# Performance work log

Measured on AMD Instinct MI355X. Metric: run time of the kernel, lower is better.

## Reference

```python
import jax, jax.numpy as jnp
import numpy as np

B, T, D, NH = 2, 2048, 2048, 16
HID = D  # hidden_dim must equal emb_dim for the source's fc2(x1) to type-check
HD = D // NH
EPS = 1e-5


def setup_inputs() -> dict:
    key = jax.random.key(0)
    ks = jax.random.split(key, 16)
    s = 0.02
    inp = {
        "x": jax.random.normal(ks[0], (B, T, D), jnp.float32),
        "Wq": jax.random.normal(ks[1], (D, D), jnp.float32) * s,
        "bq": jnp.zeros((D,), jnp.float32),
        "Wk": jax.random.normal(ks[2], (D, D), jnp.float32) * s,
        "bk": jnp.zeros((D,), jnp.float32),
        "Wv": jax.random.normal(ks[3], (D, D), jnp.float32) * s,
        "bv": jnp.zeros((D,), jnp.float32),
        "Wo": jax.random.normal(ks[4], (D, D), jnp.float32) * s,
        "bo": jnp.zeros((D,), jnp.float32),
        "scale1": jnp.ones((D,), jnp.float32),
        "scale2": jnp.ones((D,), jnp.float32),
        "W1": jax.random.normal(ks[5], (D, HID), jnp.float32) * s,
        "W2": jax.random.normal(ks[6], (D, HID), jnp.float32) * s,  # fc2: Linear(emb_dim, hidden_dim)
        "W3": jax.random.normal(ks[7], (HID, D), jnp.float32) * s,
    }
    return inp


def _rmsnorm(x, scale):
    m = jnp.mean(x * x, axis=-1, keepdims=True)
    return scale * (x * jax.lax.rsqrt(m + EPS))


def _attention(x, Wq, bq, Wk, bk, Wv, bv, Wo, bo):
    b, t, _ = x.shape
    q = (x @ Wq + bq).reshape(b, t, NH, HD)
    k = (x @ Wk + bk).reshape(b, t, NH, HD)
    v = (x @ Wv + bv).reshape(b, t, NH, HD)
    # energy: [B, H, T, T]; softmax over keys, scaled by 1/sqrt(head_dim); NO causal mask in source
    energy = jnp.einsum("bqhd,bkhd->bhqk", q, k) / jnp.sqrt(jnp.float32(HD))
    attn = jax.nn.softmax(energy, axis=-1)
    out = jnp.einsum("bhqk,bkhd->bqhd", attn, v).reshape(b, t, D)
    return out @ Wo + bo


def _ffn(x, W1, W2, W3):
    x1 = x @ W1                       # [B,T,HID]
    x2 = x1 @ W2                      # source quirk: fc2 applied to x1 (hidden_dim == emb_dim)
    return (x1 * jax.nn.sigmoid(x1) * x2) @ W3


def reference(x, Wq, bq, Wk, bk, Wv, bv, Wo, bo, scale1, scale2, W1, W2, W3):
    shortcut = x
    h = _rmsnorm(x, scale1)
    h = _attention(h, Wq, bq, Wk, bk, Wv, bv, Wo, bo)
    h = shortcut + h
    h = _rmsnorm(h, scale2)
    h = _ffn(h, W1, W2, W3)
    # source adds the ORIGINAL input again (shortcut never reassigned)
    return h + shortcut
```

## Files before the change

### kernel.cpp

```cpp
#include <hip/hip_runtime.h>

typedef __bf16 bf16x8 __attribute__((ext_vector_type(8)));
typedef __bf16 bf16x4v __attribute__((ext_vector_type(4)));
typedef float  f32x4  __attribute__((ext_vector_type(4)));

#define LDS_AS(p) ((__attribute__((address_space(3))) void*)(p))
#define GLB_AS(p) ((const __attribute__((address_space(1))) void*)(p))

struct TP { const float* s[7]; __bf16* d[7]; };
__global__ __launch_bounds__(256) void transpose_convert_all(TP p) {
  const float* __restrict__ W = p.s[blockIdx.z];
  __bf16* __restrict__ Wt = p.d[blockIdx.z];
  __shared__ float tile[32][33];
  const int tx = threadIdx.x & 31, ty = threadIdx.x >> 5;
  const int n0 = blockIdx.x * 32, k0 = blockIdx.y * 32;
#pragma unroll
  for (int j = 0; j < 4; ++j)
    tile[ty + j * 8][tx] = W[(size_t)(k0 + ty + j * 8) * 2048 + n0 + tx];
  __syncthreads();
#pragma unroll
  for (int j = 0; j < 4; ++j)
    Wt[(size_t)(n0 + ty + j * 8) * 2048 + k0 + tx] = (__bf16)tile[tx][ty + j * 8];
}

__global__ __launch_bounds__(256) void rmsnorm_k(
    const float* __restrict__ x, const float* __restrict__ scale,
    __bf16* __restrict__ out) {
  const int row = blockIdx.x, t = threadIdx.x;
  const float4* xr = (const float4*)(x + (size_t)row * 2048);
  float4 a = xr[t], b2 = xr[t + 256];
  float ss = a.x * a.x + a.y * a.y + a.z * a.z + a.w * a.w +
             b2.x * b2.x + b2.y * b2.y + b2.z * b2.z + b2.w * b2.w;
#pragma unroll
  for (int ofs = 32; ofs; ofs >>= 1) ss += __shfl_xor(ss, ofs, 64);
  __shared__ float red[4];
  if ((t & 63) == 0) red[t >> 6] = ss;
  __syncthreads();
  ss = red[0] + red[1] + red[2] + red[3];
  const float rs = rsqrtf(ss * (1.f / 2048.f) + 1e-5f);
  const float4* sr = (const float4*)scale;
  float4 s1 = sr[t], s2 = sr[t + 256];
  __bf16* orow = out + (size_t)row * 2048;
  orow[t * 4 + 0] = (__bf16)(a.x * rs * s1.x);
  orow[t * 4 + 1] = (__bf16)(a.y * rs * s1.y);
  orow[t * 4 + 2] = (__bf16)(a.z * rs * s1.z);
  orow[t * 4 + 3] = (__bf16)(a.w * rs * s1.w);
  orow[(t + 256) * 4 + 0] = (__bf16)(b2.x * rs * s2.x);
  orow[(t + 256) * 4 + 1] = (__bf16)(b2.y * rs * s2.y);
  orow[(t + 256) * 4 + 2] = (__bf16)(b2.z * rs * s2.z);
  orow[(t + 256) * 4 + 3] = (__bf16)(b2.w * rs * s2.w);
}

template <bool OUTF32, bool HASBIAS, bool HASRES, bool SILU>
__global__ __launch_bounds__(256) void gemm_bt(
    const __bf16* __restrict__ A, const __bf16* __restrict__ Bt,
    const float* __restrict__ bias, const float* __restrict__ res,
    const __bf16* __restrict__ ew, void* __restrict__ Cout,
    int M, int N, int Kd) {
  __shared__ __attribute__((aligned(16))) __bf16 As[2][128 * 32];
  __shared__ __attribute__((aligned(16))) __bf16 Bs[2][128 * 32];
  const int tid = threadIdx.x;
  const int w = tid >> 6, l = tid & 63;
  const int M0 = blockIdx.y * 128, N0 = blockIdx.x * 128;
  const int wr = w >> 1, wc = w & 1;
  const int lm = l & 15, lq = l >> 4;

  f32x4 acc[4][4];
#pragma unroll
  for (int mt = 0; mt < 4; ++mt)
#pragma unroll
    for (int nt = 0; nt < 4; ++nt)
#pragma unroll
      for (int e = 0; e < 4; ++e) acc[mt][nt][e] = 0.f;

  const int offA0 = (w * 2 + 0) * 1024 + l * 16;
  const int offA1 = (w * 2 + 1) * 1024 + l * 16;
  const int row0 = offA0 >> 6, kb0 = offA0 & 63;
  const int row1 = offA1 >> 6, kb1 = offA1 & 63;
  const int nIt = Kd >> 5;

  auto stage = [&](int k0, int bsel) {
    const char* ga0 = (const char*)(A + (size_t)(M0 + row0) * Kd + k0) + kb0;
    const char* ga1 = (const char*)(A + (size_t)(M0 + row1) * Kd + k0) + kb1;
    const char* gb0 = (const char*)(Bt + (size_t)(N0 + row0) * Kd + k0) + kb0;
    const char* gb1 = (const char*)(Bt + (size_t)(N0 + row1) * Kd + k0) + kb1;
    __builtin_amdgcn_global_load_lds(GLB_AS(ga0), LDS_AS(((char*)As[bsel]) + (w * 2 + 0) * 1024), 16, 0, 0);
    __builtin_amdgcn_global_load_lds(GLB_AS(ga1), LDS_AS(((char*)As[bsel]) + (w * 2 + 1) * 1024), 16, 0, 0);
    __builtin_amdgcn_global_load_lds(GLB_AS(gb0), LDS_AS(((char*)Bs[bsel]) + (w * 2 + 0) * 1024), 16, 0, 0);
    __builtin_amdgcn_global_load_lds(GLB_AS(gb1), LDS_AS(((char*)Bs[bsel]) + (w * 2 + 1) * 1024), 16, 0, 0);
  };

  stage(0, 0);
  for (int it = 0; it < nIt; ++it) {
    __syncthreads();
    if (it + 1 < nIt) stage((it + 1) * 32, (it + 1) & 1);
    const __bf16* Ab = As[it & 1];
    const __bf16* Bb = Bs[it & 1];
    bf16x8 af[4], bfr[4];
#pragma unroll
    for (int mt = 0; mt < 4; ++mt)
      af[mt] = *(const bf16x8*)(Ab + (wr * 64 + mt * 16 + lm) * 32 + lq * 8);
#pragma unroll
    for (int nt = 0; nt < 4; ++nt)
      bfr[nt] = *(const bf16x8*)(Bb + (wc * 64 + nt * 16 + lm) * 32 + lq * 8);
#pragma unroll
    for (int mt = 0; mt < 4; ++mt)
#pragma unroll
      for (int nt = 0; nt < 4; ++nt)
        acc[mt][nt] = __builtin_amdgcn_mfma_f32_16x16x32_bf16(af[mt], bfr[nt], acc[mt][nt], 0, 0, 0);
  }

  const int lr = lq * 4;
#pragma unroll
  for (int mt = 0; mt < 4; ++mt) {
#pragma unroll
    for (int nt = 0; nt < 4; ++nt) {
      const int col = N0 + wc * 64 + nt * 16 + lm;
      float bv = 0.f;
      if (HASBIAS) bv = bias[col];
#pragma unroll
      for (int i = 0; i < 4; ++i) {
        const int row = M0 + wr * 64 + mt * 16 + lr + i;
        const size_t off = (size_t)row * N + col;
        float v = acc[mt][nt][i] + bv;
        if (HASRES) v += res[off];
        if (SILU) {
          const float x1v = (float)ew[off];
          v = x1v * (1.f / (1.f + __expf(-x1v))) * v;
        }
        if (OUTF32) ((float*)Cout)[off] = v;
        else ((__bf16*)Cout)[off] = (__bf16)v;
      }
    }
  }
}

__global__ __launch_bounds__(256) void gemm_qkv(
    const __bf16* __restrict__ A, const __bf16* __restrict__ Bt,
    const float* __restrict__ bq, const float* __restrict__ bk,
    const float* __restrict__ bv,
    __bf16* __restrict__ Qout, __bf16* __restrict__ Kout,
    __bf16* __restrict__ Vtout, int Kd) {
  __shared__ __attribute__((aligned(16))) __bf16 As[2][128 * 32];
  __shared__ __attribute__((aligned(16))) __bf16 Bs[2][128 * 32];
  const int tid = threadIdx.x;
  const int w = tid >> 6, l = tid & 63;
  const int M0 = blockIdx.y * 128, N0 = blockIdx.x * 128;
  const int wr = w >> 1, wc = w & 1;
  const int lm = l & 15, lq = l >> 4;

  f32x4 acc[4][4];
#pragma unroll
  for (int mt = 0; mt < 4; ++mt)
#pragma unroll
    for (int nt = 0; nt < 4; ++nt)
#pragma unroll
      for (int e = 0; e < 4; ++e) acc[mt][nt][e] = 0.f;

  const int offA0 = (w * 2 + 0) * 1024 + l * 16;
  const int offA1 = (w * 2 + 1) * 1024 + l * 16;
  const int row0 = offA0 >> 6, kb0 = offA0 & 63;
  const int row1 = offA1 >> 6, kb1 = offA1 & 63;
  const int nIt = Kd >> 5;

  auto stage = [&](int k0, int bsel) {
    const char* ga0 = (const char*)(A + (size_t)(M0 + row0) * Kd + k0) + kb0;
    const char* ga1 = (const char*)(A + (size_t)(M0 + row1) * Kd + k0) + kb1;
    const char* gb0 = (const char*)(Bt + (size_t)(N0 + row0) * Kd + k0) + kb0;
    const char* gb1 = (const char*)(Bt + (size_t)(N0 + row1) * Kd + k0) + kb1;
    __builtin_amdgcn_global_load_lds(GLB_AS(ga0), LDS_AS(((char*)As[bsel]) + (w * 2 + 0) * 1024), 16, 0, 0);
    __builtin_amdgcn_global_load_lds(GLB_AS(ga1), LDS_AS(((char*)As[bsel]) + (w * 2 + 1) * 1024), 16, 0, 0);
    __builtin_amdgcn_global_load_lds(GLB_AS(gb0), LDS_AS(((char*)Bs[bsel]) + (w * 2 + 0) * 1024), 16, 0, 0);
    __builtin_amdgcn_global_load_lds(GLB_AS(gb1), LDS_AS(((char*)Bs[bsel]) + (w * 2 + 1) * 1024), 16, 0, 0);
  };

  stage(0, 0);
  for (int it = 0; it < nIt; ++it) {
    __syncthreads();
    if (it + 1 < nIt) stage((it + 1) * 32, (it + 1) & 1);
    const __bf16* Ab = As[it & 1];
    const __bf16* Bb = Bs[it & 1];
    bf16x8 af[4], bfr[4];
#pragma unroll
    for (int mt = 0; mt < 4; ++mt)
      af[mt] = *(const bf16x8*)(Ab + (wr * 64 + mt * 16 + lm) * 32 + lq * 8);
#pragma unroll
    for (int nt = 0; nt < 4; ++nt)
      bfr[nt] = *(const bf16x8*)(Bb + (wc * 64 + nt * 16 + lm) * 32 + lq * 8);
#pragma unroll
    for (int mt = 0; mt < 4; ++mt)
#pragma unroll
      for (int nt = 0; nt < 4; ++nt)
        acc[mt][nt] = __builtin_amdgcn_mfma_f32_16x16x32_bf16(af[mt], bfr[nt], acc[mt][nt], 0, 0, 0);
  }

  const int lr = lq * 4;
  const int seg = N0 >> 11;
  const int nbase = N0 & 2047;
  const float* bb = (seg == 0) ? bq : ((seg == 1) ? bk : bv);
  if (seg < 2) {
    __bf16* dst = (seg == 0) ? Qout : Kout;
#pragma unroll
    for (int mt = 0; mt < 4; ++mt) {
#pragma unroll
      for (int nt = 0; nt < 4; ++nt) {
        const int col = nbase + wc * 64 + nt * 16 + lm;
        const float bvv = bb[col];
#pragma unroll
        for (int i = 0; i < 4; ++i) {
          const int row = M0 + wr * 64 + mt * 16 + lr + i;
          dst[(size_t)row * 2048 + col] = (__bf16)(acc[mt][nt][i] + bvv);
        }
      }
    }
  } else {
#pragma unroll
    for (int mt = 0; mt < 4; ++mt) {
#pragma unroll
      for (int nt = 0; nt < 4; ++nt) {
        const int col = nbase + wc * 64 + nt * 16 + lm;
        const float bvv = bb[col];
        const int rw0 = M0 + wr * 64 + mt * 16 + lr;
        const int bidx = rw0 >> 11, tok = rw0 & 2047;
        bf16x4v pk;
#pragma unroll
        for (int i = 0; i < 4; ++i) pk[i] = (__bf16)(acc[mt][nt][i] + bvv);
        *(bf16x4v*)(Vtout + ((size_t)(bidx * 2048 + col)) * 2048 + tok) = pk;
      }
    }
  }
}

__global__ __launch_bounds__(256, 2) void attn_mfma(
    const __bf16* __restrict__ Q, const __bf16* __restrict__ K,
    const __bf16* __restrict__ Vt, __bf16* __restrict__ O) {
  __shared__ __attribute__((aligned(16))) char KsL[2][16 * 1024];
  __shared__ __attribute__((aligned(16))) char VsL[2][16 * 1024];

  const int t = threadIdx.x;
  const int w = t >> 6, l = t & 63;
  const int lm = l & 15, quad = l >> 4;
  const int h = blockIdx.y, b = blockIdx.z;
  const int q0 = blockIdx.x * 128;
  const size_t Ds = 2048;
  const size_t hoff = (size_t)h * 128;
  const size_t bbase = (size_t)b * 2048;
  const int sl16 = ((lm << 2) | quad) * 16;
  const float SCL = 0.08838834764831845f * 1.4426950408889634f;

  const int krow = l >> 2, kcol = (l & 3) * 8;
  const int vth = l & 3, vd = l >> 2;

  bf16x8 qf[2][4];
#pragma unroll
  for (int ntq = 0; ntq < 2; ++ntq)
#pragma unroll
    for (int ks = 0; ks < 4; ++ks)
      qf[ntq][ks] = *(const bf16x8*)(Q + (bbase + q0 + w * 32 + ntq * 16 + lm) * Ds + hoff + ks * 32 + quad * 8);

  f32x4 oacc[2][8];
#pragma unroll
  for (int ntq = 0; ntq < 2; ++ntq)
#pragma unroll
    for (int nv = 0; nv < 8; ++nv)
#pragma unroll
      for (int e = 0; e < 4; ++e) oacc[ntq][nv][e] = 0.f;
  float lpart[2] = {0.f, 0.f};

  bf16x8 vreg[4];

  auto loadV = [&](int kt) {
#pragma unroll
    for (int i = 0; i < 4; ++i) {
      const int chunk = w * 4 + i;
      const int nv = chunk >> 1, c = chunk & 1;
      vreg[i] = *(const bf16x8*)(Vt + (bbase + hoff + nv * 16 + vd) * Ds + kt + c * 32 + vth * 8);
    }
  };
  auto stageK = [&](int kt, char* Kb) {
#pragma unroll
    for (int i = 0; i < 4; ++i) {
      const __bf16* src = K + (bbase + kt + i * 16 + krow) * Ds + hoff + w * 32 + kcol;
      __builtin_amdgcn_global_load_lds(GLB_AS(src), LDS_AS(Kb + (i * 4 + w) * 1024), 16, 0, 0);
    }
  };
  auto writeV = [&](char* Vb) {
    const int s0off = ((vd << 2) | ((vth & 1) * 2)) * 16 + (vth >> 1) * 8;
#pragma unroll
    for (int i = 0; i < 4; ++i) {
      char* base = Vb + (w * 4 + i) * 1024;
      uint4 u = *(const uint4*)&vreg[i];
      *(uint2*)(base + s0off) = make_uint2(u.x, u.y);
      *(uint2*)(base + s0off + 16) = make_uint2(u.z, u.w);
    }
  };

  loadV(0);
  stageK(0, KsL[0]);
  writeV(VsL[0]);

  for (int it = 0; it < 32; ++it) {
    __syncthreads();
    const int cur = it & 1;
    const bool more = (it + 1) < 32;
    if (more) { loadV((it + 1) * 64); stageK((it + 1) * 64, KsL[(it + 1) & 1]); }

    const char* Kb = KsL[cur];
    const char* Vb = VsL[cur];

    f32x4 st[4][2];
#pragma unroll
    for (int mtk = 0; mtk < 4; ++mtk)
#pragma unroll
      for (int ntq = 0; ntq < 2; ++ntq)
#pragma unroll
        for (int e = 0; e < 4; ++e) st[mtk][ntq][e] = 0.f;
#pragma unroll
    for (int ks = 0; ks < 4; ++ks) {
#pragma unroll
      for (int mtk = 0; mtk < 4; ++mtk) {
        bf16x8 kf = *(const bf16x8*)(Kb + (mtk * 4 + ks) * 1024 + sl16);
        st[mtk][0] = __builtin_amdgcn_mfma_f32_16x16x32_bf16(kf, qf[0][ks], st[mtk][0], 0, 0, 0);
        st[mtk][1] = __builtin_amdgcn_mfma_f32_16x16x32_bf16(kf, qf[1][ks], st[mtk][1], 0, 0, 0);
      }
    }

#pragma unroll
    for (int c = 0; c < 2; ++c) {
      bf16x8 pf[2];
#pragma unroll
      for (int ntq = 0; ntq < 2; ++ntq) {
#pragma unroll
        for (int half = 0; half < 2; ++half) {
          const f32x4 sv = st[c * 2 + half][ntq];
#pragma unroll
          for (int r = 0; r < 4; ++r) {
            const float p = exp2f(sv[r] * SCL);
            const __bf16 pb = (__bf16)p;
            pf[ntq][half * 4 + r] = pb;
            lpart[ntq] += (float)pb;
          }
        }
      }
#pragma unroll
      for (int nv = 0; nv < 8; ++nv) {
        bf16x8 vf = *(const bf16x8*)(Vb + (nv * 2 + c) * 1024 + sl16);
        oacc[0][nv] = __builtin_amdgcn_mfma_f32_16x16x32_bf16(pf[0], vf, oacc[0][nv], 0, 0, 0);
        oacc[1][nv] = __builtin_amdgcn_mfma_f32_16x16x32_bf16(pf[1], vf, oacc[1][nv], 0, 0, 0);
      }
    }

    if (more) writeV(VsL[(it + 1) & 1]);
  }

  float linv[2];
#pragma unroll
  for (int ntq = 0; ntq < 2; ++ntq) {
    float v = lpart[ntq];
    v += __shfl_xor(v, 16, 64);
    v += __shfl_xor(v, 32, 64);
    linv[ntq] = 1.f / v;
  }
  float oinv[2][4];
#pragma unroll
  for (int ntq = 0; ntq < 2; ++ntq)
#pragma unroll
    for (int r = 0; r < 4; ++r)
      oinv[ntq][r] = __shfl(linv[ntq], quad * 4 + r, 64);

#pragma unroll
  for (int ntq = 0; ntq < 2; ++ntq)
#pragma unroll
    for (int nv = 0; nv < 8; ++nv)
#pragma unroll
      for (int r = 0; r < 4; ++r) {
        const int qrow = q0 + w * 32 + ntq * 16 + quad * 4 + r;
        O[(bbase + qrow) * Ds + hoff + nv * 16 + lm] = (__bf16)(oacc[ntq][nv][r] * oinv[ntq][r]);
      }
}

extern "C" void kernel_launch(void* const* d_in, const int* in_sizes, int n_in,
                              void* d_out, int out_size, void* d_ws, size_t ws_size,
                              hipStream_t stream) {
  const float* x      = (const float*)d_in[0];
  const float* Wq     = (const float*)d_in[1];
  const float* bq     = (const float*)d_in[2];
  const float* Wk     = (const float*)d_in[3];
  const float* bk     = (const float*)d_in[4];
  const float* Wv     = (const float*)d_in[5];
  const float* bv     = (const float*)d_in[6];
  const float* Wo     = (const float*)d_in[7];
  const float* bo     = (const float*)d_in[8];
  const float* scale1 = (const float*)d_in[9];
  const float* scale2 = (const float*)d_in[10];
  const float* W1     = (const float*)d_in[11];
  const float* W2     = (const float*)d_in[12];
  const float* W3     = (const float*)d_in[13];

  const int M = 4096, N = 2048, Kd = 2048;
  char* ws = (char*)d_ws;
  const size_t WT_B = (size_t)2048 * 2048 * 2;
  const size_t ACT_B = (size_t)4096 * 2048 * 2;
  __bf16* wt[7];
  size_t off = 0;
  for (int i = 0; i < 7; ++i) { wt[i] = (__bf16*)(ws + off); off += WT_B; }
  __bf16* hn1  = (__bf16*)(ws + off); off += ACT_B;
  __bf16* Qb   = (__bf16*)(ws + off); off += ACT_B;
  __bf16* Kb   = (__bf16*)(ws + off); off += ACT_B;
  __bf16* VtG  = (__bf16*)(ws + off); off += ACT_B;
  __bf16* attn = (__bf16*)(ws + off); off += ACT_B;
  __bf16* hn2  = (__bf16*)(ws + off); off += ACT_B;
  __bf16* x1b  = (__bf16*)(ws + off); off += ACT_B;
  __bf16* fmb  = (__bf16*)(ws + off); off += ACT_B;

  dim3 tb(256);
  {
    TP p;
    p.s[0] = Wq; p.s[1] = Wk; p.s[2] = Wv; p.s[3] = Wo; p.s[4] = W1; p.s[5] = W2; p.s[6] = W3;
    for (int i = 0; i < 7; ++i) p.d[i] = wt[i];
    transpose_convert_all<<<dim3(64, 64, 7), tb, 0, stream>>>(p);
  }

  rmsnorm_k<<<4096, tb, 0, stream>>>(x, scale1, hn1);

  gemm_qkv<<<dim3(6144 / 128, M / 128), tb, 0, stream>>>(
      hn1, wt[0], bq, bk, bv, Qb, Kb, VtG, Kd);

  dim3 ag(2048 / 128, 16, 2);
  attn_mfma<<<ag, tb, 0, stream>>>(Qb, Kb, VtG, attn);

  dim3 gg(N / 128, M / 128);
  gemm_bt<true, true, true, false><<<gg, tb, 0, stream>>>(attn, wt[3], bo, x, nullptr, d_out, M, N, Kd);

  rmsnorm_k<<<4096, tb, 0, stream>>>((const float*)d_out, scale2, hn2);

  gemm_bt<false, false, false, false><<<gg, tb, 0, stream>>>(hn2, wt[4], nullptr, nullptr, nullptr, x1b, M, N, Kd);
  gemm_bt<false, false, false, true><<<gg, tb, 0, stream>>>(x1b, wt[5], nullptr, nullptr, x1b, fmb, M, N, Kd);
  gemm_bt<true, false, true, false><<<gg, tb, 0, stream>>>(fmb, wt[6], nullptr, x, nullptr, d_out, M, N, Kd);
}
```

Measured before the change: 649.2 us.

## Fold W1·W2 into one interleaved FFN GEMM with fused SiLU epilogue

Reassociates the FFN so that x2 = h·(W1·W2). A 2048³ weight GEMM computes W1·W2 on every call, and its columns are interleaved with W1 into a single 4096-wide B matrix. One GEMM then produces x1 and x2 tiles together and applies the SiLU gating in its epilogue through an LDS exchange, which removes the dependent second GEMM and the x1 round trip through global memory. The price is an extra weight GEMM plus an interleave copy, and x2 is now computed from a bf16-rounded W12, which slightly changes numerics. Separately, the QKV GEMM moves to 256x128 tiles with 4x8 MFMA accumulators per wave, to get more reuse of each B tile.

```diff
diff --git a/kernel.cpp b/kernel.cpp
--- a/kernel.cpp
+++ b/kernel.cpp
@@ -7,7 +7,7 @@
 #define LDS_AS(p) ((__attribute__((address_space(3))) void*)(p))
 #define GLB_AS(p) ((const __attribute__((address_space(1))) void*)(p))
 
-struct TP { const float* s[7]; __bf16* d[7]; };
+struct TP { const float* s[7]; __bf16* d[7]; __bf16* w1b; };
 __global__ __launch_bounds__(256) void transpose_convert_all(TP p) {
   const float* __restrict__ W = p.s[blockIdx.z];
   __bf16* __restrict__ Wt = p.d[blockIdx.z];
@@ -21,6 +21,21 @@
 #pragma unroll
   for (int j = 0; j < 4; ++j)
     Wt[(size_t)(n0 + ty + j * 8) * 2048 + k0 + tx] = (__bf16)tile[tx][ty + j * 8];
+  if (blockIdx.z == 4) {
+#pragma unroll
+    for (int j = 0; j < 4; ++j)
+      p.w1b[(size_t)(k0 + ty + j * 8) * 2048 + n0 + tx] = (__bf16)tile[ty + j * 8][tx];
+  }
+}
+
+__global__ __launch_bounds__(256) void ffn_interleave(
+    const __bf16* __restrict__ W1t, const __bf16* __restrict__ W12t,
+    __bf16* __restrict__ BtFFN) {
+  const int r = blockIdx.x;
+  const int t = r >> 7, c = r & 127;
+  const __bf16* src = (c < 64) ? (W1t + (size_t)(t * 64 + c) * 2048)
+                               : (W12t + (size_t)(t * 64 + (c - 64)) * 2048);
+  ((uint4*)(BtFFN + (size_t)r * 2048))[threadIdx.x] = ((const uint4*)src)[threadIdx.x];
 }
 
 __global__ __launch_bounds__(256) void rmsnorm_k(
@@ -51,12 +66,11 @@
   orow[(t + 256) * 4 + 3] = (__bf16)(b2.w * rs * s2.w);
 }
 
-template <bool OUTF32, bool HASBIAS, bool HASRES, bool SILU>
+template <bool OUTF32, bool HASBIAS, bool HASRES>
 __global__ __launch_bounds__(256) void gemm_bt(
     const __bf16* __restrict__ A, const __bf16* __restrict__ Bt,
     const float* __restrict__ bias, const float* __restrict__ res,
-    const __bf16* __restrict__ ew, void* __restrict__ Cout,
-    int M, int N, int Kd) {
+    void* __restrict__ Cout, int M, int N, int Kd) {
   __shared__ __attribute__((aligned(16))) __bf16 As[2][128 * 32];
   __shared__ __attribute__((aligned(16))) __bf16 Bs[2][128 * 32];
   const int tid = threadIdx.x;
@@ -73,21 +87,18 @@
 #pragma unroll
       for (int e = 0; e < 4; ++e) acc[mt][nt][e] = 0.f;
 
-  const int offA0 = (w * 2 + 0) * 1024 + l * 16;
-  const int offA1 = (w * 2 + 1) * 1024 + l * 16;
-  const int row0 = offA0 >> 6, kb0 = offA0 & 63;
-  const int row1 = offA1 >> 6, kb1 = offA1 & 63;
+  const int srow = l >> 2, sk = (l & 3) * 16;
   const int nIt = Kd >> 5;
 
   auto stage = [&](int k0, int bsel) {
-    const char* ga0 = (const char*)(A + (size_t)(M0 + row0) * Kd + k0) + kb0;
-    const char* ga1 = (const char*)(A + (size_t)(M0 + row1) * Kd + k0) + kb1;
-    const char* gb0 = (const char*)(Bt + (size_t)(N0 + row0) * Kd + k0) + kb0;
-    const char* gb1 = (const char*)(Bt + (size_t)(N0 + row1) * Kd + k0) + kb1;
-    __builtin_amdgcn_global_load_lds(GLB_AS(ga0), LDS_AS(((char*)As[bsel]) + (w * 2 + 0) * 1024), 16, 0, 0);
-    __builtin_amdgcn_global_load_lds(GLB_AS(ga1), LDS_AS(((char*)As[bsel]) + (w * 2 + 1) * 1024), 16, 0, 0);
-    __builtin_amdgcn_global_load_lds(GLB_AS(gb0), LDS_AS(((char*)Bs[bsel]) + (w * 2 + 0) * 1024), 16, 0, 0);
-    __builtin_amdgcn_global_load_lds(GLB_AS(gb1), LDS_AS(((char*)Bs[bsel]) + (w * 2 + 1) * 1024), 16, 0, 0);
+#pragma unroll
+    for (int i = 0; i < 2; ++i) {
+      const int c = w * 2 + i;
+      const char* ga = (const char*)(A + (size_t)(M0 + c * 16 + srow) * Kd + k0) + sk;
+      const char* gb = (const char*)(Bt + (size_t)(N0 + c * 16 + srow) * Kd + k0) + sk;
+      __builtin_amdgcn_global_load_lds(GLB_AS(ga), LDS_AS(((char*)As[bsel]) + c * 1024), 16, 0, 0);
+      __builtin_amdgcn_global_load_lds(GLB_AS(gb), LDS_AS(((char*)Bs[bsel]) + c * 1024), 16, 0, 0);
+    }
   };
 
   stage(0, 0);
@@ -124,10 +135,6 @@
         const size_t off = (size_t)row * N + col;
         float v = acc[mt][nt][i] + bv;
         if (HASRES) v += res[off];
-        if (SILU) {
-          const float x1v = (float)ew[off];
-          v = x1v * (1.f / (1.f + __expf(-x1v))) * v;
-        }
         if (OUTF32) ((float*)Cout)[off] = v;
         else ((__bf16*)Cout)[off] = (__bf16)v;
       }
@@ -141,37 +148,37 @@
     const float* __restrict__ bv,
     __bf16* __restrict__ Qout, __bf16* __restrict__ Kout,
     __bf16* __restrict__ Vtout, int Kd) {
-  __shared__ __attribute__((aligned(16))) __bf16 As[2][128 * 32];
+  __shared__ __attribute__((aligned(16))) __bf16 As[2][256 * 32];
   __shared__ __attribute__((aligned(16))) __bf16 Bs[2][128 * 32];
   const int tid = threadIdx.x;
   const int w = tid >> 6, l = tid & 63;
-  const int M0 = blockIdx.y * 128, N0 = blockIdx.x * 128;
-  const int wr = w >> 1, wc = w & 1;
+  const int M0 = blockIdx.y * 256, N0 = blockIdx.x * 128;
   const int lm = l & 15, lq = l >> 4;
 
-  f32x4 acc[4][4];
+  f32x4 acc[4][8];
 #pragma unroll
   for (int mt = 0; mt < 4; ++mt)
 #pragma unroll
-    for (int nt = 0; nt < 4; ++nt)
+    for (int nt = 0; nt < 8; ++nt)
 #pragma unroll
       for (int e = 0; e < 4; ++e) acc[mt][nt][e] = 0.f;
 
-  const int offA0 = (w * 2 + 0) * 1024 + l * 16;
-  const int offA1 = (w * 2 + 1) * 1024 + l * 16;
-  const int row0 = offA0 >> 6, kb0 = offA0 & 63;
-  const int row1 = offA1 >> 6, kb1 = offA1 & 63;
+  const int srow = l >> 2, sk = (l & 3) * 16;
   const int nIt = Kd >> 5;
 
   auto stage = [&](int k0, int bsel) {
-    const char* ga0 = (const char*)(A + (size_t)(M0 + row0) * Kd + k0) + kb0;
-    const char* ga1 = (const char*)(A + (size_t)(M0 + row1) * Kd + k0) + kb1;
-    const char* gb0 = (const char*)(Bt + (size_t)(N0 + row0) * Kd + k0) + kb0;
-    const char* gb1 = (const char*)(Bt + (size_t)(N0 + row1) * Kd + k0) + kb1;
-    __builtin_amdgcn_global_load_lds(GLB_AS(ga0), LDS_AS(((char*)As[bsel]) + (w * 2 + 0) * 1024), 16, 0, 0);
-    __builtin_amdgcn_global_load_lds(GLB_AS(ga1), LDS_AS(((char*)As[bsel]) + (w * 2 + 1) * 1024), 16, 0, 0);
-    __builtin_amdgcn_global_load_lds(GLB_AS(gb0), LDS_AS(((char*)Bs[bsel]) + (w * 2 + 0) * 1024), 16, 0, 0);
-    __builtin_amdgcn_global_load_lds(GLB_AS(gb1), LDS_AS(((char*)Bs[bsel]) + (w * 2 + 1) * 1024), 16, 0, 0);
+#pragma unroll
+    for (int i = 0; i < 4; ++i) {
+      const int c = w * 4 + i;
+      const char* ga = (const char*)(A + (size_t)(M0 + c * 16 + srow) * Kd + k0) + sk;
+      __builtin_amdgcn_global_load_lds(GLB_AS(ga), LDS_AS(((char*)As[bsel]) + c * 1024), 16, 0, 0);
+    }
+#pragma unroll
+    for (int i = 0; i < 2; ++i) {
+      const int c = w * 2 + i;
+      const char* gb = (const char*)(Bt + (size_t)(N0 + c * 16 + srow) * Kd + k0) + sk;
+      __builtin_amdgcn_global_load_lds(GLB_AS(gb), LDS_AS(((char*)Bs[bsel]) + c * 1024), 16, 0, 0);
+    }
   };
 
   stage(0, 0);
@@ -180,17 +187,17 @@
     if (it + 1 < nIt) stage((it + 1) * 32, (it + 1) & 1);
     const __bf16* Ab = As[it & 1];
     const __bf16* Bb = Bs[it & 1];
-    bf16x8 af[4], bfr[4];
-#pragma unroll
-    for (int mt = 0; mt < 4; ++mt)
-      af[mt] = *(const bf16x8*)(Ab + (wr * 64 + mt * 16 + lm) * 32 + lq * 8);
-#pragma unroll
-    for (int nt = 0; nt < 4; ++nt)
-      bfr[nt] = *(const bf16x8*)(Bb + (wc * 64 + nt * 16 + lm) * 32 + lq * 8);
-#pragma unroll
-    for (int mt = 0; mt < 4; ++mt)
-#pragma unroll
-      for (int nt = 0; nt < 4; ++nt)
+    bf16x8 af[4], bfr[8];
+#pragma unroll
+    for (int mt = 0; mt < 4; ++mt)
+      af[mt] = *(const bf16x8*)(Ab + (w * 64 + mt * 16 + lm) * 32 + lq * 8);
+#pragma unroll
+    for (int nt = 0; nt < 8; ++nt)
+      bfr[nt] = *(const bf16x8*)(Bb + (nt * 16 + lm) * 32 + lq * 8);
+#pragma unroll
+    for (int mt = 0; mt < 4; ++mt)
+#pragma unroll
+      for (int nt = 0; nt < 8; ++nt)
         acc[mt][nt] = __builtin_amdgcn_mfma_f32_16x16x32_bf16(af[mt], bfr[nt], acc[mt][nt], 0, 0, 0);
   }
 
@@ -203,29 +210,114 @@
 #pragma unroll
     for (int mt = 0; mt < 4; ++mt) {
 #pragma unroll
+      for (int nt = 0; nt < 8; ++nt) {
+        const int col = nbase + nt * 16 + lm;
+        const float bvv = bb[col];
+#pragma unroll
+        for (int i = 0; i < 4; ++i) {
+          const int row = M0 + w * 64 + mt * 16 + lr + i;
+          dst[(size_t)row * 2048 + col] = (__bf16)(acc[mt][nt][i] + bvv);
+        }
+      }
+    }
+  } else {
+#pragma unroll
+    for (int mt = 0; mt < 4; ++mt) {
+#pragma unroll
+      for (int nt = 0; nt < 8; ++nt) {
+        const int col = nbase + nt * 16 + lm;
+        const float bvv = bb[col];
+        const int rw0 = M0 + w * 64 + mt * 16 + lr;
+        const int bidx = rw0 >> 11, tok = rw0 & 2047;
+        bf16x4v pk;
+#pragma unroll
+        for (int i = 0; i < 4; ++i) pk[i] = (__bf16)(acc[mt][nt][i] + bvv);
+        *(bf16x4v*)(Vtout + ((size_t)(bidx * 2048 + col)) * 2048 + tok) = pk;
+      }
+    }
+  }
+}
+
+__global__ __launch_bounds__(256) void gemm_ffn(
+    const __bf16* __restrict__ A, const __bf16* __restrict__ Bt,
+    __bf16* __restrict__ FM, int Kd) {
+  __shared__ __attribute__((aligned(16))) char SM[32768];
+  const int tid = threadIdx.x;
+  const int w = tid >> 6, l = tid & 63;
+  const int M0 = blockIdx.y * 128, N0 = blockIdx.x * 128;
+  const int wr = w >> 1, wc = w & 1;
+  const int lm = l & 15, lq = l >> 4;
+
+  f32x4 acc[4][4];
+#pragma unroll
+  for (int mt = 0; mt < 4; ++mt)
+#pragma unroll
+    for (int nt = 0; nt < 4; ++nt)
+#pragma unroll
+      for (int e = 0; e < 4; ++e) acc[mt][nt][e] = 0.f;
+
+  const int srow = l >> 2, sk = (l & 3) * 16;
+  const int nIt = Kd >> 5;
+
+  auto stage = [&](int k0, int bsel) {
+    char* Abuf = SM + bsel * 8192;
+    char* Bbuf = SM + 16384 + bsel * 8192;
+#pragma unroll
+    for (int i = 0; i < 2; ++i) {
+      const int c = w * 2 + i;
+      const char* ga = (const char*)(A + (size_t)(M0 + c * 16 + srow) * Kd + k0) + sk;
+      const char* gb = (const char*)(Bt + (size_t)(N0 + c * 16 + srow) * Kd + k0) + sk;
+      __builtin_amdgcn_global_load_lds(GLB_AS(ga), LDS_AS(Abuf + c * 1024), 16, 0, 0);
+      __builtin_amdgcn_global_load_lds(GLB_AS(gb), LDS_AS(Bbuf + c * 1024), 16, 0, 0);
+    }
+  };
+
+  stage(0, 0);
+  for (int it = 0; it < nIt; ++it) {
+    __syncthreads();
+    if (it + 1 < nIt) stage((it + 1) * 32, (it + 1) & 1);
+    const __bf16* Ab = (const __bf16*)(SM + (it & 1) * 8192);
+    const __bf16* Bb = (const __bf16*)(SM + 16384 + (it & 1) * 8192);
+    bf16x8 af[4], bfr[4];
+#pragma unroll
+    for (int mt = 0; mt < 4; ++mt)
+      af[mt] = *(const bf16x8*)(Ab + (wr * 64 + mt * 16 + lm) * 32 + lq * 8);
+#pragma unroll
+    for (int nt = 0; nt < 4; ++nt)
+      bfr[nt] = *(const bf16x8*)(Bb + (wc * 64 + nt * 16 + lm) * 32 + lq * 8);
+#pragma unroll
+    for (int mt = 0; mt < 4; ++mt)
+#pragma unroll
+      for (int nt = 0; nt < 4; ++nt)
+        acc[mt][nt] = __builtin_amdgcn_mfma_f32_16x16x32_bf16(af[mt], bfr[nt], acc[mt][nt], 0, 0, 0);
+  }
+
+  __syncthreads();
+  if (wc == 1) {
+    float* dst = (float*)(SM + wr * 16384);
+#pragma unroll
+    for (int mt = 0; mt < 4; ++mt)
+#pragma unroll
+      for (int nt = 0; nt < 4; ++nt)
+        *(f32x4*)(dst + ((mt * 4 + nt) * 64 + l) * 4) = acc[mt][nt];
+  }
+  __syncthreads();
+  if (wc == 0) {
+    const float* src = (const float*)(SM + wr * 16384);
+    const int lr = lq * 4;
+#pragma unroll
+    for (int mt = 0; mt < 4; ++mt) {
+#pragma unroll
       for (int nt = 0; nt < 4; ++nt) {
-        const int col = nbase + wc * 64 + nt * 16 + lm;
-        const float bvv = bb[col];
+        const f32x4 x2 = *(const f32x4*)(src + ((mt * 4 + nt) * 64 + l) * 4);
+        const int col = (N0 >> 1) + nt * 16 + lm;
 #pragma unroll
         for (int i = 0; i < 4; ++i) {
           const int row = M0 + wr * 64 + mt * 16 + lr + i;
-          dst[(size_t)row * 2048 + col] = (__bf16)(acc[mt][nt][i] + bvv);
+          const float x1 = acc[mt][nt][i];
+          const float v = x1 * (1.f / (1.f + __expf(-x1))) * x2[i];
+          FM[(size_t)row * 2048 + col] = (__bf16)v;
         }
-      }
-    }
-  } else {
-#pragma unroll
-    for (int mt = 0; mt < 4; ++mt) {
-#pragma unroll
-      for (int nt = 0; nt < 4; ++nt) {
-        const int col = nbase + wc * 64 + nt * 16 + lm;
-        const float bvv = bb[col];
-        const int rw0 = M0 + wr * 64 + mt * 16 + lr;
-        const int bidx = rw0 >> 11, tok = rw0 & 2047;
-        bf16x4v pk;
-#pragma unroll
-        for (int i = 0; i < 4; ++i) pk[i] = (__bf16)(acc[mt][nt][i] + bvv);
-        *(bf16x4v*)(Vtout + ((size_t)(bidx * 2048 + col)) * 2048 + tok) = pk;
       }
     }
   }
@@ -404,37 +496,44 @@
   __bf16* wt[7];
   size_t off = 0;
   for (int i = 0; i < 7; ++i) { wt[i] = (__bf16*)(ws + off); off += WT_B; }
-  __bf16* hn1  = (__bf16*)(ws + off); off += ACT_B;
-  __bf16* Qb   = (__bf16*)(ws + off); off += ACT_B;
-  __bf16* Kb   = (__bf16*)(ws + off); off += ACT_B;
-  __bf16* VtG  = (__bf16*)(ws + off); off += ACT_B;
-  __bf16* attn = (__bf16*)(ws + off); off += ACT_B;
-  __bf16* hn2  = (__bf16*)(ws + off); off += ACT_B;
-  __bf16* x1b  = (__bf16*)(ws + off); off += ACT_B;
-  __bf16* fmb  = (__bf16*)(ws + off); off += ACT_B;
+  __bf16* hn1   = (__bf16*)(ws + off); off += ACT_B;
+  __bf16* Qb    = (__bf16*)(ws + off); off += ACT_B;
+  __bf16* Kb    = (__bf16*)(ws + off); off += ACT_B;
+  __bf16* VtG   = (__bf16*)(ws + off); off += ACT_B;
+  __bf16* attn  = (__bf16*)(ws + off); off += ACT_B;
+  __bf16* hn2   = (__bf16*)(ws + off); off += ACT_B;
+  __bf16* BtFFN = (__bf16*)(ws + off); off += ACT_B;
+  __bf16* fmb   = (__bf16*)(ws + off); off += ACT_B;
+  __bf16* W1b  = Qb;
+  __bf16* W12t = Kb;
 
   dim3 tb(256);
   {
     TP p;
     p.s[0] = Wq; p.s[1] = Wk; p.s[2] = Wv; p.s[3] = Wo; p.s[4] = W1; p.s[5] = W2; p.s[6] = W3;
     for (int i = 0; i < 7; ++i) p.d[i] = wt[i];
+    p.w1b = W1b;
     transpose_convert_all<<<dim3(64, 64, 7), tb, 0, stream>>>(p);
   }
 
+  gemm_bt<false, false, false><<<dim3(16, 16), tb, 0, stream>>>(
+      wt[5], W1b, nullptr, nullptr, W12t, 2048, 2048, 2048);
+  ffn_interleave<<<4096, tb, 0, stream>>>(wt[4], W12t, BtFFN);
+
   rmsnorm_k<<<4096, tb, 0, stream>>>(x, scale1, hn1);
 
-  gemm_qkv<<<dim3(6144 / 128, M / 128), tb, 0, stream>>>(
+  gemm_qkv<<<dim3(6144 / 128, M / 256), tb, 0, stream>>>(
       hn1, wt[0], bq, bk, bv, Qb, Kb, VtG, Kd);
 
   dim3 ag(2048 / 128, 16, 2);
   attn_mfma<<<ag, tb, 0, stream>>>(Qb, Kb, VtG, attn);
 
   dim3 gg(N / 128, M / 128);
-  gemm_bt<true, true, true, false><<<gg, tb, 0, stream>>>(attn, wt[3], bo, x, nullptr, d_out, M, N, Kd);
+  gemm_bt<true, true, true><<<gg, tb, 0, stream>>>(attn, wt[3], bo, x, d_out, M, N, Kd);
 
   rmsnorm_k<<<4096, tb, 0, stream>>>((const float*)d_out, scale2, hn2);
 
-  gemm_bt<false, false, false, false><<<gg, tb, 0, stream>>>(hn2, wt[4], nullptr, nullptr, nullptr, x1b, M, N, Kd);
-  gemm_bt<false, false, false, true><<<gg, tb, 0, stream>>>(x1b, wt[5], nullptr, nullptr, x1b, fmb, M, N, Kd);
-  gemm_bt<true, false, true, false><<<gg, tb, 0, stream>>>(fmb, wt[6], nullptr, x, nullptr, d_out, M, N, Kd);
-}
+  gemm_ffn<<<dim3(32, 32), tb, 0, stream>>>(hn2, BtFFN, fmb, Kd);
+
+  gemm_bt<true, false, true><<<gg, tb, 0, stream>>>(fmb, wt[6], nullptr, x, d_out, M, N, Kd);
+}
```

New measurement: 737.8 us. 13.6% more time.
